# Kernel tuning notes

Measured on AMD Instinct MI355X. Metric: run time of the kernel, lower is better.

Reference implementation:

```python
import jax, jax.numpy as jnp
import numpy as np
from math import sqrt

B, S, E, H = 2, 2048, 1024, 16

def setup_inputs() -> dict:
    key = jax.random.key(0)
    k1, k2, k3, k4, k5 = jax.random.split(key, 5)
    bound_in = 1.0 / sqrt(E)
    return {
        "inputs": jax.random.normal(k1, (B, S, E), dtype=jnp.float32),
        "W_in": jax.random.uniform(k2, (3 * E, E), dtype=jnp.float32, minval=-bound_in, maxval=bound_in),
        "b_in": jax.random.uniform(k3, (3 * E,), dtype=jnp.float32, minval=-bound_in, maxval=bound_in),
        "W_out": jax.random.uniform(k4, (E, E), dtype=jnp.float32, minval=-bound_in, maxval=bound_in),
        "b_out": jax.random.uniform(k5, (E,), dtype=jnp.float32, minval=-bound_in, maxval=bound_in),
    }

def reference(inputs, W_in, b_in, W_out, b_out):
    # Eval-mode forward (dropout is identity when not training).
    b, s, e = inputs.shape
    hd = e // H
    qkv = jnp.einsum('bse,fe->bsf', inputs, W_in) + b_in  # [B,S,3E]
    q, k, v = jnp.split(qkv, 3, axis=-1)
    # [B,S,E] -> [B,H,S,hd]
    to_heads = lambda t: t.reshape(b, s, H, hd).transpose(0, 2, 1, 3)
    q, k, v = to_heads(q), to_heads(k), to_heads(v)
    scores = jnp.einsum('bhqd,bhkd->bhqk', q, k) / jnp.sqrt(jnp.float32(hd))
    causal = jnp.tril(jnp.ones((s, s), dtype=bool))
    scores = jnp.where(causal, scores, -jnp.inf)
    attn = jax.nn.softmax(scores, axis=-1)  # stable max-subtract softmax, same math
    out = jnp.einsum('bhqk,bhkd->bhqd', attn, v)  # [B,H,S,hd]
    out = out.transpose(0, 2, 1, 3).reshape(b, s, e)
    return jnp.einsum('bse,fe->bsf', out, W_out) + b_out
```

## Files before the change

### kernel.cpp

```cpp
#include <hip/hip_runtime.h>
#include <hip/hip_bf16.h>
#include <stdint.h>

#define SS 2048
#define EE 1024
#define HH 16
#define HD 64

#define QSCALE 0.1803368801111137f

typedef __attribute__((ext_vector_type(8))) short short8;
typedef __attribute__((ext_vector_type(4))) float f32x4;

__device__ __forceinline__ short f2bf(float f) {
  union { float f; uint32_t u; } x; x.f = f;
  uint32_t r = x.u + 0x7fffu + ((x.u >> 16) & 1u);
  return (short)(r >> 16);
}

__device__ __forceinline__ uint32_t pk_bf16(float a, float b) {
#if __has_builtin(__builtin_amdgcn_cvt_pk_bf16_f32)
  typedef __attribute__((ext_vector_type(2))) __bf16 bf16x2_t;
  union { bf16x2_t v; uint32_t u; } x;
  x.v = __builtin_amdgcn_cvt_pk_bf16_f32(a, b);
  return x.u;
#else
  return (uint32_t)(uint16_t)f2bf(a) | ((uint32_t)(uint16_t)f2bf(b) << 16);
#endif
}

__device__ __forceinline__ void async_cp16(const void* g, void* l) {
  __builtin_amdgcn_global_load_lds((const __attribute__((address_space(1))) void*)g,
                                   (__attribute__((address_space(3))) void*)l, 16, 0, 0);
}

#define N4_X  1048576
#define N4_W1 786432
#define N4_W2 262144
__global__ __launch_bounds__(256) void cvt_all(
    const float* __restrict__ x, const float* __restrict__ w1,
    const float* __restrict__ w2,
    short* __restrict__ xb, short* __restrict__ w1b, short* __restrict__ w2b)
{
  int i = blockIdx.x * 256 + threadIdx.x;
  const float* src; short* dst; int off;
  if (i < N4_X)            { src = x;  dst = xb;  off = i; }
  else if (i < N4_X+N4_W1) { src = w1; dst = w1b; off = i - N4_X; }
  else                     { src = w2; dst = w2b; off = i - N4_X - N4_W1; }
  float4 v = *(const float4*)&src[(size_t)off * 4];
  uint2 pk;
  pk.x = pk_bf16(v.x, v.y);
  pk.y = pk_bf16(v.z, v.w);
  *(uint2*)&dst[(size_t)off * 4] = pk;
}

__global__ __launch_bounds__(256) void gemm_qkv(
    const short* __restrict__ A, const short* __restrict__ Bw,
    const float* __restrict__ bias,
    short* __restrict__ qw, short* __restrict__ kw, short* __restrict__ vw,
    int M, int N, int K)
{
  __shared__ short smem[17408];
  const int tid = threadIdx.x;
  const int lane = tid & 63;
  const int wv = tid >> 6;
  const int wm = (wv >> 1) * 64;
  const int wn = (wv & 1) * 64;
  const int t = lane >> 4;
  const int lr = lane & 15;
  const int bm = blockIdx.y * 128;
  const int bn = blockIdx.x * 128;

  f32x4 acc[4][4];
  #pragma unroll
  for (int i = 0; i < 4; ++i)
    #pragma unroll
    for (int j = 0; j < 4; ++j) acc[i][j] = (f32x4){0.f, 0.f, 0.f, 0.f};

  auto stage = [&](int buf, int k0) {
    short* sA = smem + buf * 8192;
    short* sB = smem + buf * 8192 + 4096;
    #pragma unroll
    for (int it = 0; it < 2; ++it) {
      int c = it * 256 + wv * 64 + lane;
      int row = c >> 2;
      int ch = (c & 3) * 8;
      async_cp16(&A[(size_t)(bm + row) * K + k0 + ch],
                 (char*)sA + (size_t)(it * 256 + wv * 64) * 16);
      async_cp16(&Bw[(size_t)(bn + row) * K + k0 + ch],
                 (char*)sB + (size_t)(it * 256 + wv * 64) * 16);
    }
  };

  const int nk = K >> 5;
  stage(0, 0);
  __syncthreads();

  for (int k = 0; k < nk; ++k) {
    if (k + 1 < nk) stage((k + 1) & 1, (k + 1) << 5);
    const short* cA = smem + (k & 1) * 8192;
    const short* cB = smem + (k & 1) * 8192 + 4096;
    short8 af[4], bfr[4];
    #pragma unroll
    for (int i = 0; i < 4; ++i) af[i] = *(const short8*)&cA[(wm + i*16 + lr)*32 + t*8];
    #pragma unroll
    for (int j = 0; j < 4; ++j) bfr[j] = *(const short8*)&cB[(wn + j*16 + lr)*32 + t*8];
    #pragma unroll
    for (int i = 0; i < 4; ++i)
      #pragma unroll
      for (int j = 0; j < 4; ++j)
        acc[i][j] = __builtin_amdgcn_mfma_f32_16x16x32_bf16(af[i], bfr[j], acc[i][j], 0, 0, 0);
    __syncthreads();
  }

  short* vx = smem;
  const bool isV = (bn >= 2048);
  const bool isQ = (bn < 1024);
  int b_ = bm >> 11;
  int s0 = bm & 2047;
  if (isV) {
    #pragma unroll
    for (int i = 0; i < 4; ++i) {
      int row0 = wm + i*16 + t*4;
      #pragma unroll
      for (int j = 0; j < 4; ++j) {
        int cl = wn + j*16 + lr;
        float bv = bias[bn + cl];
        #pragma unroll
        for (int r = 0; r < 4; ++r)
          vx[cl*136 + row0 + r] = f2bf(acc[i][j][r] + bv);
      }
    }
    __syncthreads();
    int h0 = (bn - 2048) >> 6;
    #pragma unroll
    for (int it = 0; it < 8; ++it) {
      int cc = it * 256 + tid;
      int cl = cc >> 4;
      int ck = cc & 15;
      int h = h0 + (cl >> 6);
      int d = cl & 63;
      *(uint4*)&vw[((size_t)(b_*HH + h)*HD + d)*SS + s0 + ck*8] =
          *(const uint4*)&vx[cl*136 + ck*8];
    }
  } else {
    #pragma unroll
    for (int i = 0; i < 4; ++i) {
      int row0 = wm + i*16 + t*4;
      #pragma unroll
      for (int j = 0; j < 4; ++j) {
        int cl = wn + j*16 + lr;
        float bv = bias[bn + cl];
        #pragma unroll
        for (int r = 0; r < 4; ++r) {
          float v = acc[i][j][r] + bv;
          if (isQ) v *= QSCALE;
          vx[(row0 + r)*136 + cl] = f2bf(v);
        }
      }
    }
    __syncthreads();
    short* dst = isQ ? qw : kw;
    int h0 = (bn & 1023) >> 6;
    #pragma unroll
    for (int it = 0; it < 8; ++it) {
      int cc = it * 256 + tid;
      int row = cc >> 4;
      int ck = cc & 15;
      int h = h0 + (ck >> 3);
      int d0 = (ck & 7) * 8;
      *(uint4*)&dst[((size_t)(b_*HH + h)*SS + s0 + row)*HD + d0] =
          *(const uint4*)&vx[row*136 + ck*8];
    }
  }
}

__global__ __launch_bounds__(256) void gemm_out(
    const short* __restrict__ A, const short* __restrict__ Bw,
    const float* __restrict__ bias,
    float* __restrict__ C,
    int M, int N, int K)
{
  __shared__ short smem[12288];
  const int tid = threadIdx.x;
  const int lane = tid & 63;
  const int wv = tid >> 6;
  const int wm = (wv >> 1) * 32;
  const int wn = (wv & 1) * 64;
  const int t = lane >> 4;
  const int lr = lane & 15;
  const int bm = blockIdx.y * 64;
  const int bn = blockIdx.x * 128;

  f32x4 acc[2][4];
  #pragma unroll
  for (int i = 0; i < 2; ++i)
    #pragma unroll
    for (int j = 0; j < 4; ++j) acc[i][j] = (f32x4){0.f, 0.f, 0.f, 0.f};

  auto stage = [&](int buf, int k0) {
    short* sA = smem + buf * 6144;
    short* sB = smem + buf * 6144 + 2048;
    {
      int c = wv * 64 + lane;
      int row = c >> 2;
      int ch = (c & 3) * 8;
      async_cp16(&A[(size_t)(bm + row) * K + k0 + ch],
                 (char*)sA + (size_t)(wv * 64) * 16);
    }
    #pragma unroll
    for (int it = 0; it < 2; ++it) {
      int c = it * 256 + wv * 64 + lane;
      int row = c >> 2;
      int ch = (c & 3) * 8;
      async_cp16(&Bw[(size_t)(bn + row) * K + k0 + ch],
                 (char*)sB + (size_t)(it * 256 + wv * 64) * 16);
    }
  };

  const int nk = K >> 5;
  stage(0, 0);
  __syncthreads();

  for (int k = 0; k < nk; ++k) {
    if (k + 1 < nk) stage((k + 1) & 1, (k + 1) << 5);
    const short* cA = smem + (k & 1) * 6144;
    const short* cB = smem + (k & 1) * 6144 + 2048;
    short8 af[2], bfr[4];
    #pragma unroll
    for (int i = 0; i < 2; ++i) af[i] = *(const short8*)&cA[(wm + i*16 + lr)*32 + t*8];
    #pragma unroll
    for (int j = 0; j < 4; ++j) bfr[j] = *(const short8*)&cB[(wn + j*16 + lr)*32 + t*8];
    #pragma unroll
    for (int i = 0; i < 2; ++i)
      #pragma unroll
      for (int j = 0; j < 4; ++j)
        acc[i][j] = __builtin_amdgcn_mfma_f32_16x16x32_bf16(af[i], bfr[j], acc[i][j], 0, 0, 0);
    __syncthreads();
  }

  #pragma unroll
  for (int i = 0; i < 2; ++i) {
    int row0 = bm + wm + i*16 + t*4;
    #pragma unroll
    for (int j = 0; j < 4; ++j) {
      int col = bn + wn + j*16 + lr;
      float bv = bias[col];
      #pragma unroll
      for (int r = 0; r < 4; ++r)
        C[(size_t)(row0 + r) * N + col] = acc[i][j][r] + bv;
    }
  }
}

template<int MODE, typename TA>
__global__ __launch_bounds__(256) void gemm_bt(
    const TA* __restrict__ A, const float* __restrict__ Bw,
    const float* __restrict__ bias,
    float* __restrict__ C,
    short* __restrict__ qw, short* __restrict__ kw, short* __restrict__ vw,
    int M, int N, int K)
{
  __shared__ short sA[128*32];
  __shared__ short sB[128*32];
  const int tid = threadIdx.x;
  const int lane = tid & 63;
  const int wv = tid >> 6;
  const int wm = (wv >> 1) * 64;
  const int wn = (wv & 1) * 64;
  const int t = lane >> 4;
  const int lr = lane & 15;
  const int bm = blockIdx.y * 128;
  const int bn = blockIdx.x * 128;

  f32x4 acc[4][4];
  #pragma unroll
  for (int i = 0; i < 4; ++i)
    #pragma unroll
    for (int j = 0; j < 4; ++j) acc[i][j] = (f32x4){0.f, 0.f, 0.f, 0.f};

  for (int k0 = 0; k0 < K; k0 += 32) {
    __syncthreads();
    if constexpr (sizeof(TA) == 4) {
      #pragma unroll
      for (int it = 0; it < 4; ++it) {
        int c = it * 256 + tid;
        int row = c >> 3, ch = (c & 7) * 4;
        float4 va = *(const float4*)&A[(size_t)(bm + row)*K + k0 + ch];
        uint2 pk; pk.x = pk_bf16(va.x, va.y); pk.y = pk_bf16(va.z, va.w);
        *(uint2*)&sA[row*32 + ch] = pk;
      }
    } else {
      #pragma unroll
      for (int it = 0; it < 2; ++it) {
        int c = it * 256 + tid;
        int row = c >> 2, ch = (c & 3) * 8;
        *(uint4*)&sA[row*32 + ch] = *(const uint4*)&A[(size_t)(bm + row)*K + k0 + ch];
      }
    }
    #pragma unroll
    for (int it = 0; it < 4; ++it) {
      int c = it * 256 + tid;
      int row = c >> 3, ch = (c & 7) * 4;
      float4 vb = *(const float4*)&Bw[(size_t)(bn + row)*K + k0 + ch];
      uint2 pk; pk.x = pk_bf16(vb.x, vb.y); pk.y = pk_bf16(vb.z, vb.w);
      *(uint2*)&sB[row*32 + ch] = pk;
    }
    __syncthreads();
    short8 af[4], bfr[4];
    #pragma unroll
    for (int i = 0; i < 4; ++i) af[i] = *(const short8*)&sA[(wm + i*16 + lr)*32 + t*8];
    #pragma unroll
    for (int j = 0; j < 4; ++j) bfr[j] = *(const short8*)&sB[(wn + j*16 + lr)*32 + t*8];
    #pragma unroll
    for (int i = 0; i < 4; ++i)
      #pragma unroll
      for (int j = 0; j < 4; ++j)
        acc[i][j] = __builtin_amdgcn_mfma_f32_16x16x32_bf16(af[i], bfr[j], acc[i][j], 0, 0, 0);
  }

  #pragma unroll
  for (int i = 0; i < 4; ++i) {
    int row0 = bm + wm + i*16 + t*4;
    #pragma unroll
    for (int j = 0; j < 4; ++j) {
      int col = bn + wn + j*16 + lr;
      float bv = bias[col];
      #pragma unroll
      for (int r = 0; r < 4; ++r) {
        float v = acc[i][j][r] + bv;
        int rr = row0 + r;
        if (MODE == 0) {
          C[(size_t)rr * N + col] = v;
        } else {
          int which = col >> 10;
          int e = col & 1023;
          int h = e >> 6, d = e & 63;
          int b_ = rr >> 11, s = rr & 2047;
          if (which == 0)
            qw[((size_t)(b_*HH + h)*SS + s)*HD + d] = f2bf(v * QSCALE);
          else if (which == 1)
            kw[((size_t)(b_*HH + h)*SS + s)*HD + d] = f2bf(v);
          else
            vw[((size_t)(b_*HH + h)*HD + d)*SS + s] = f2bf(v);
        }
      }
    }
  }
}

__global__ __launch_bounds__(512) void attn_kernel(
    const short* __restrict__ Q, const short* __restrict__ K,
    const short* __restrict__ Vt, short* __restrict__ O)
{
  __shared__ short sK[2][128*64];
  __shared__ short sV[2][64*128];
  __shared__ short sP[8][16*64];
  const int tid = threadIdx.x;
  const int lane = tid & 63;
  const int w = tid >> 6;
  const int t = lane >> 4;
  const int lr = lane & 15;
  const int blk = blockIdx.x;
  const int qt = (blk < 256) ? (blk >> 5) : (15 - ((blk - 256) >> 5));
  const int bh = blk & 31;
  const int b = bh >> 4, h = bh & 15;
  const short* Qb = Q  + (size_t)bh * SS * HD;
  const short* Kb = K  + (size_t)bh * SS * HD;
  const short* Vb = Vt + (size_t)bh * HD * SS;
  const int qrow0 = qt * 128 + w * 16;
  short* sPw = sP[w];

  auto stage = [&](int buf, int kb) {
    #pragma unroll
    for (int it2 = 0; it2 < 2; ++it2) {
      int s = it2 * 512 + tid;
      int krow = s >> 3;
      int kcc = (s & 7) ^ (krow & 7);
      async_cp16(&Kb[(size_t)(kb + krow) * HD + kcc * 8],
                 (char*)sK[buf] + (size_t)(it2 * 512 + w * 64) * 16);
      int d = s >> 4;
      int vcc = (s & 15) ^ (d & 15);
      async_cp16(&Vb[(size_t)d * SS + kb + vcc * 8],
                 (char*)sV[buf] + (size_t)(it2 * 512 + w * 64) * 16);
    }
  };

  short8 qf[2];
  #pragma unroll
  for (int st = 0; st < 2; ++st)
    qf[st] = *(const short8*)&Qb[(size_t)(qrow0 + lr) * HD + st*32 + t*8];

  f32x4 o[4];
  #pragma unroll
  for (int jd = 0; jd < 4; ++jd) o[jd] = (f32x4){0.f, 0.f, 0.f, 0.f};
  float l = 0.f;

  const int niter = qt + 1;
  stage(0, 0);
  __syncthreads();
  int cur = 0;

  #pragma unroll 1
  for (int it = 0; it < niter; ++it) {
    const int kb = it * 128;
    if (it + 1 < niter) stage(cur ^ 1, kb + 128);
    const short* sKc = sK[cur];
    const short* sVc = sV[cur];

    f32x4 sc[8];
    #pragma unroll
    for (int c = 0; c < 8; ++c) sc[c] = (f32x4){0.f,0.f,0.f,0.f};
    #pragma unroll
    for (int c = 0; c < 8; ++c) {
      int krow = c*16 + lr;
      #pragma unroll
      for (int st = 0; st < 2; ++st) {
        int slot = krow*8 + ((st*4 + t) ^ (krow & 7));
        short8 kf = *(const short8*)&sKc[slot*8];
        sc[c] = __builtin_amdgcn_mfma_f32_16x16x32_bf16(kf, qf[st], sc[c], 0, 0, 0);
      }
    }

    if (it == niter - 1) {
      int qg = qrow0 + lr;
      #pragma unroll
      for (int c = 0; c < 8; ++c)
        #pragma unroll
        for (int r = 0; r < 4; ++r)
          if (kb + c*16 + t*4 + r > qg) sc[c][r] = -1e30f;
    }

    float rs = 0.f;
    #pragma unroll
    for (int c = 0; c < 8; ++c)
      #pragma unroll
      for (int r = 0; r < 4; ++r) {
        sc[c][r] = exp2f(sc[c][r]);
        rs += sc[c][r];
      }
    rs += __shfl_xor(rs, 16);
    rs += __shfl_xor(rs, 32);
    l += rs;

    #pragma unroll
    for (int hf = 0; hf < 2; ++hf) {
      #pragma unroll
      for (int c2 = 0; c2 < 4; ++c2) {
        int c = hf*4 + c2;
        uint2 pk2;
        pk2.x = pk_bf16(sc[c][0], sc[c][1]);
        pk2.y = pk_bf16(sc[c][2], sc[c][3]);
        int chunk = 2*c2 + (t >> 1);
        *(uint2*)&sPw[lr*64 + ((chunk ^ (lr & 7)) * 8) + (t & 1) * 4] = pk2;
      }
      #pragma unroll
      for (int fl = 0; fl < 2; ++fl) {
        int chunk = 4*fl + t;
        short8 pf = *(const short8*)&sPw[lr*64 + ((chunk ^ (lr & 7)) * 8)];
        int f = hf*2 + fl;
        #pragma unroll
        for (int jd = 0; jd < 4; ++jd) {
          int d = jd*16 + lr;
          int vslot = d*16 + ((f*4 + t) ^ (d & 15));
          short8 vf = *(const short8*)&sVc[vslot*8];
          o[jd] = __builtin_amdgcn_mfma_f32_16x16x32_bf16(vf, pf, o[jd], 0, 0, 0);
        }
      }
    }

    __syncthreads();
    cur ^= 1;
  }

  float linv = 1.0f / l;
  size_t rowoff = ((size_t)(b * SS + qrow0 + lr)) * EE + h * HD;
  #pragma unroll
  for (int jd = 0; jd < 4; ++jd) {
    uint2 pw;
    pw.x = pk_bf16(o[jd][0] * linv, o[jd][1] * linv);
    pw.y = pk_bf16(o[jd][2] * linv, o[jd][3] * linv);
    *(uint2*)&O[rowoff + jd*16 + t*4] = pw;
  }
}

extern "C" void kernel_launch(void* const* d_in, const int* in_sizes, int n_in,
                              void* d_out, int out_size, void* d_ws, size_t ws_size,
                              hipStream_t stream) {
  const float* X     = (const float*)d_in[0];
  const float* W_in  = (const float*)d_in[1];
  const float* b_in  = (const float*)d_in[2];
  const float* W_out = (const float*)d_in[3];
  const float* b_out = (const float*)d_in[4];
  float* out = (float*)d_out;

  char* ws = (char*)d_ws;
  const size_t MB = 1024 * 1024;
  const int M = 2 * SS;

  if (ws_size >= 48 * MB) {
    short* Xb   = (short*)(ws);
    short* Wb1  = (short*)(ws + 8  * MB);
    short* Wb2  = (short*)(ws + 14 * MB);
    short* q_ws = (short*)(ws + 16 * MB);
    short* k_ws = (short*)(ws + 24 * MB);
    short* v_ws = (short*)(ws + 32 * MB);
    short* attn = (short*)(ws + 40 * MB);

    cvt_all<<<8192, 256, 0, stream>>>(X, W_in, W_out, Xb, Wb1, Wb2);
    gemm_qkv<<<dim3(24, 32), 256, 0, stream>>>(
        Xb, Wb1, b_in, q_ws, k_ws, v_ws, M, 3 * EE, EE);
    attn_kernel<<<dim3(512), 512, 0, stream>>>(q_ws, k_ws, v_ws, attn);
    gemm_out<<<dim3(8, 64), 256, 0, stream>>>(
        attn, Wb2, b_out, out, M, EE, EE);
  } else {
    short* q_ws = (short*)(ws);
    short* k_ws = (short*)(ws + 8  * MB);
    short* v_ws = (short*)(ws + 16 * MB);
    short* attn = (short*)(ws + 24 * MB);

    gemm_bt<1, float><<<dim3(24, 32), 256, 0, stream>>>(
        X, W_in, b_in, nullptr, q_ws, k_ws, v_ws, M, 3 * EE, EE);
    attn_kernel<<<dim3(512), 512, 0, stream>>>(q_ws, k_ws, v_ws, attn);
    gemm_bt<0, short><<<dim3(8, 32), 256, 0, stream>>>(
        attn, W_out, b_out, out, nullptr, nullptr, nullptr, M, EE, EE);
  }
}
```

Before: 193.1 us.

## Keep P in registers by permuting V's key order instead of LDS round-trip

Removes the per-wave shared-memory staging of the softmax probabilities. The PV MFMA now takes P directly from the QK accumulator registers, and the V tensor is written by both projection paths in a permuted key order within each 128-key block so that the register layout matches. The change also swaps exp2f for the hardware exp2 builtin, adds s_setprio around the MFMA blocks, and simplifies the swizzle XOR terms. The cost is a more intricate index permutation in the V writers, which must stay consistent across both projection variants.

```diff
diff --git a/kernel.cpp b/kernel.cpp
--- a/kernel.cpp
+++ b/kernel.cpp
@@ -28,6 +28,12 @@
   return (uint32_t)(uint16_t)f2bf(a) | ((uint32_t)(uint16_t)f2bf(b) << 16);
 #endif
 }
+
+#if __has_builtin(__builtin_amdgcn_exp2f)
+#define EXP2F __builtin_amdgcn_exp2f
+#else
+#define EXP2F exp2f
+#endif
 
 __device__ __forceinline__ void async_cp16(const void* g, void* l) {
   __builtin_amdgcn_global_load_lds((const __attribute__((address_space(1))) void*)g,
@@ -140,8 +146,12 @@
       int ck = cc & 15;
       int h = h0 + (cl >> 6);
       int d = cl & 63;
-      *(uint4*)&vw[((size_t)(b_*HH + h)*HD + d)*SS + s0 + ck*8] =
-          *(const uint4*)&vx[cl*136 + ck*8];
+      int f = ck >> 2, tt = ck & 3;
+      const short* src = &vx[cl*136 + 32*f + 4*tt];
+      uint2 lo = *(const uint2*)src;
+      uint2 hi = *(const uint2*)(src + 16);
+      uint4 val; val.x = lo.x; val.y = lo.y; val.z = hi.x; val.w = hi.y;
+      *(uint4*)&vw[((size_t)(b_*HH + h)*HD + d)*SS + s0 + ck*8] = val;
     }
   } else {
     #pragma unroll
@@ -341,8 +351,11 @@
             qw[((size_t)(b_*HH + h)*SS + s)*HD + d] = f2bf(v * QSCALE);
           else if (which == 1)
             kw[((size_t)(b_*HH + h)*SS + s)*HD + d] = f2bf(v);
-          else
-            vw[((size_t)(b_*HH + h)*HD + d)*SS + s] = f2bf(v);
+          else {
+            int k7 = s & 127;
+            int sp = (k7 & 0x60) | ((k7 & 0x0C) << 1) | ((k7 & 0x10) >> 2) | (k7 & 3);
+            vw[((size_t)(b_*HH + h)*HD + d)*SS + (s & ~127) + sp] = f2bf(v);
+          }
         }
       }
     }
@@ -355,7 +368,6 @@
 {
   __shared__ short sK[2][128*64];
   __shared__ short sV[2][64*128];
-  __shared__ short sP[8][16*64];
   const int tid = threadIdx.x;
   const int lane = tid & 63;
   const int w = tid >> 6;
@@ -369,7 +381,6 @@
   const short* Kb = K  + (size_t)bh * SS * HD;
   const short* Vb = Vt + (size_t)bh * HD * SS;
   const int qrow0 = qt * 128 + w * 16;
-  short* sPw = sP[w];
 
   auto stage = [&](int buf, int kb) {
     #pragma unroll
@@ -411,16 +422,18 @@
     f32x4 sc[8];
     #pragma unroll
     for (int c = 0; c < 8; ++c) sc[c] = (f32x4){0.f,0.f,0.f,0.f};
+    __builtin_amdgcn_s_setprio(1);
     #pragma unroll
     for (int c = 0; c < 8; ++c) {
       int krow = c*16 + lr;
       #pragma unroll
       for (int st = 0; st < 2; ++st) {
-        int slot = krow*8 + ((st*4 + t) ^ (krow & 7));
+        int slot = krow*8 + ((st*4 + t) ^ (lr & 7));
         short8 kf = *(const short8*)&sKc[slot*8];
         sc[c] = __builtin_amdgcn_mfma_f32_16x16x32_bf16(kf, qf[st], sc[c], 0, 0, 0);
       }
     }
+    __builtin_amdgcn_s_setprio(0);
 
     if (it == niter - 1) {
       int qg = qrow0 + lr;
@@ -436,38 +449,31 @@
     for (int c = 0; c < 8; ++c)
       #pragma unroll
       for (int r = 0; r < 4; ++r) {
-        sc[c][r] = exp2f(sc[c][r]);
+        sc[c][r] = EXP2F(sc[c][r]);
         rs += sc[c][r];
       }
     rs += __shfl_xor(rs, 16);
     rs += __shfl_xor(rs, 32);
     l += rs;
 
-    #pragma unroll
-    for (int hf = 0; hf < 2; ++hf) {
-      #pragma unroll
-      for (int c2 = 0; c2 < 4; ++c2) {
-        int c = hf*4 + c2;
-        uint2 pk2;
-        pk2.x = pk_bf16(sc[c][0], sc[c][1]);
-        pk2.y = pk_bf16(sc[c][2], sc[c][3]);
-        int chunk = 2*c2 + (t >> 1);
-        *(uint2*)&sPw[lr*64 + ((chunk ^ (lr & 7)) * 8) + (t & 1) * 4] = pk2;
-      }
-      #pragma unroll
-      for (int fl = 0; fl < 2; ++fl) {
-        int chunk = 4*fl + t;
-        short8 pf = *(const short8*)&sPw[lr*64 + ((chunk ^ (lr & 7)) * 8)];
-        int f = hf*2 + fl;
-        #pragma unroll
-        for (int jd = 0; jd < 4; ++jd) {
-          int d = jd*16 + lr;
-          int vslot = d*16 + ((f*4 + t) ^ (d & 15));
-          short8 vf = *(const short8*)&sVc[vslot*8];
-          o[jd] = __builtin_amdgcn_mfma_f32_16x16x32_bf16(vf, pf, o[jd], 0, 0, 0);
-        }
-      }
-    }
+    __builtin_amdgcn_s_setprio(1);
+    #pragma unroll
+    for (int f = 0; f < 4; ++f) {
+      union { uint32_t u[4]; short8 s8; } up;
+      up.u[0] = pk_bf16(sc[2*f  ][0], sc[2*f  ][1]);
+      up.u[1] = pk_bf16(sc[2*f  ][2], sc[2*f  ][3]);
+      up.u[2] = pk_bf16(sc[2*f+1][0], sc[2*f+1][1]);
+      up.u[3] = pk_bf16(sc[2*f+1][2], sc[2*f+1][3]);
+      short8 pf = up.s8;
+      #pragma unroll
+      for (int jd = 0; jd < 4; ++jd) {
+        int d = jd*16 + lr;
+        int vslot = d*16 + ((f*4 + t) ^ lr);
+        short8 vf = *(const short8*)&sVc[vslot*8];
+        o[jd] = __builtin_amdgcn_mfma_f32_16x16x32_bf16(vf, pf, o[jd], 0, 0, 0);
+      }
+    }
+    __builtin_amdgcn_s_setprio(0);
 
     __syncthreads();
     cur ^= 1;
```

After: 179.5 us. 1.08x faster.
